# Kernel tuning notes

Hardware: AMD Instinct MI355X
Metric: run time of the kernel (lower is better)

The kernel has to match this reference:

```python
import jax, jax.numpy as jnp
import numpy as np

B, T, D, H = 2, 2048, 1024, 16
DH = D // H  # 64


def setup_inputs() -> dict:
    key = jax.random.key(0)
    ks = jax.random.split(key, 6)
    s = 1.0 / np.sqrt(D)
    return {
        "x": jax.random.normal(ks[0], (B, T, D), dtype=jnp.float32),
        "Wq": jax.random.normal(ks[1], (D, D), dtype=jnp.float32) * s,
        "Wk": jax.random.normal(ks[2], (D, D), dtype=jnp.float32) * s,
        "Wv": jax.random.normal(ks[3], (D, D), dtype=jnp.float32) * s,
        "Wo": jax.random.normal(ks[4], (D, D), dtype=jnp.float32) * s,
        "bo": jnp.zeros((D,), dtype=jnp.float32),
    }


def reference(x, Wq, Wk, Wv, Wo, bo):
    b, t, _ = x.shape
    # projections (torch Linear: x @ W.T; here W stored as [d_in, d_out])
    q = (x @ Wq).reshape(b, t, H, DH).transpose(0, 2, 1, 3)  # [b,H,t,dh]
    k = (x @ Wk).reshape(b, t, H, DH).transpose(0, 2, 1, 3)
    v = (x @ Wv).reshape(b, t, H, DH).transpose(0, 2, 1, 3)
    scores = jnp.einsum("bhqd,bhkd->bhqk", q, k) / np.sqrt(DH).astype(np.float32)
    causal = jnp.tril(jnp.ones((t, t), dtype=bool))  # True = keep
    scores = jnp.where(causal, scores, -jnp.inf)
    weights = jax.nn.softmax(scores, axis=-1)
    ctx = jnp.einsum("bhqk,bhkd->bhqd", weights, v)
    ctx = ctx.transpose(0, 2, 1, 3).reshape(b, t, D)
    return ctx @ Wo + bo
```

## Files before the change

kernel.cpp:

```cpp
#include <hip/hip_runtime.h>


typedef unsigned short u16;
typedef __attribute__((ext_vector_type(8))) short short8;
typedef __attribute__((ext_vector_type(4))) short short4_t;
typedef __attribute__((ext_vector_type(4))) float f32x4;

#define B_ 2
#define T_ 2048
#define D_ 1024
#define H_ 16
#define DH_ 64
#define M_ (B_ * T_)
#define SCALE_LOG2E 0.18033688011112042f
#define NEG_BIG -3.0e4f

#define GLOAD16(g, l)                                                     \
  __builtin_amdgcn_global_load_lds(                                       \
      (const __attribute__((address_space(1))) void*)(g),                 \
      (__attribute__((address_space(3))) void*)(l), 16, 0, 0)

__device__ __forceinline__ u16 f2bf(float f) {
  union { float f; unsigned u; } v; v.f = f;
  unsigned r = v.u + 0x7fffu + ((v.u >> 16) & 1u);
  return (u16)(r >> 16);
}
__device__ __forceinline__ u16 f2bf_trunc(float f) {
  union { float f; unsigned u; } v; v.f = f;
  return (u16)(v.u >> 16);
}
__device__ __forceinline__ float exp2_raw(float x) {
  float r;
  asm volatile("v_exp_f32 %0, %1" : "=v"(r) : "v"(x));
  return r;
}

__global__ __launch_bounds__(256) void cvt_x(const float* __restrict__ x,
                                             u16* __restrict__ xb) {
  const int i = (blockIdx.x * 256 + threadIdx.x) * 8;
  float4 a = *(const float4*)(x + i);
  float4 b = *(const float4*)(x + i + 4);
  short8 o;
  o[0] = (short)f2bf(a.x); o[1] = (short)f2bf(a.y);
  o[2] = (short)f2bf(a.z); o[3] = (short)f2bf(a.w);
  o[4] = (short)f2bf(b.x); o[5] = (short)f2bf(b.y);
  o[6] = (short)f2bf(b.z); o[7] = (short)f2bf(b.w);
  *(short8*)(xb + i) = o;
}

__global__ __launch_bounds__(256) void transpose_w(
    const float* __restrict__ w0, const float* __restrict__ w1,
    const float* __restrict__ w2, const float* __restrict__ w3,
    u16* __restrict__ outT) {
  __shared__ u16 Tl[64][72];
  const int z = blockIdx.z;
  const float* src = (z == 0) ? w0 : (z == 1) ? w1 : (z == 2) ? w2 : w3;
  const int r0 = blockIdx.y * 64, c0 = blockIdx.x * 64;
  const int tid = threadIdx.x;
  const int rr = tid >> 2, cc = (tid & 3) * 16;

  const float* p = src + (size_t)(r0 + rr) * D_ + c0 + cc;
  float4 f0 = *(const float4*)p;
  float4 f1 = *(const float4*)(p + 4);
  float4 f2 = *(const float4*)(p + 8);
  float4 f3 = *(const float4*)(p + 12);
  Tl[rr][cc + 0] = f2bf(f0.x); Tl[rr][cc + 1] = f2bf(f0.y);
  Tl[rr][cc + 2] = f2bf(f0.z); Tl[rr][cc + 3] = f2bf(f0.w);
  Tl[rr][cc + 4] = f2bf(f1.x); Tl[rr][cc + 5] = f2bf(f1.y);
  Tl[rr][cc + 6] = f2bf(f1.z); Tl[rr][cc + 7] = f2bf(f1.w);
  Tl[rr][cc + 8] = f2bf(f2.x); Tl[rr][cc + 9] = f2bf(f2.y);
  Tl[rr][cc +10] = f2bf(f2.z); Tl[rr][cc +11] = f2bf(f2.w);
  Tl[rr][cc +12] = f2bf(f3.x); Tl[rr][cc +13] = f2bf(f3.y);
  Tl[rr][cc +14] = f2bf(f3.z); Tl[rr][cc +15] = f2bf(f3.w);
  __syncthreads();

  u16* o = outT + (size_t)z * D_ * D_ + (size_t)(c0 + rr) * D_ + r0 + cc;
  short8 x0, x1;
#pragma unroll
  for (int i = 0; i < 8; i++) x0[i] = (short)Tl[cc + i][rr];
#pragma unroll
  for (int i = 0; i < 8; i++) x1[i] = (short)Tl[cc + 8 + i][rr];
  *(short8*)o = x0;
  *(short8*)(o + 8) = x1;
}

__global__ __launch_bounds__(256) void qkv_gemm(
    const u16* __restrict__ x, const u16* __restrict__ wT,
    u16* __restrict__ qkv) {
  __shared__ u16 As[128][32];
  __shared__ u16 Bs[128][32];

  const int z = blockIdx.z;
  const u16* W = wT + (size_t)z * D_ * D_;
  u16* out = qkv + (size_t)z * M_ * D_;
  const int n0 = blockIdx.x * 128;
  const int m0 = blockIdx.y * 128;
  const int tid = threadIdx.x;
  const int lane = tid & 63, w = tid >> 6;
  const int quad = lane >> 4, l16 = lane & 15;
  const int wr = w >> 1, wc = w & 1;

  f32x4 acc[4][4] = {};
  const int grow = w * 16 + (lane >> 2);
  const int gcol = (lane & 3) * 8;
  u16* lA = (u16*)As + w * 512;
  u16* lB = (u16*)Bs + w * 512;

  for (int k0 = 0; k0 < D_; k0 += 32) {
    const u16* gA = x + (size_t)(m0 + grow) * D_ + k0 + gcol;
    const u16* gB = W + (size_t)(n0 + grow) * D_ + k0 + gcol;
    GLOAD16(gA, lA);
    GLOAD16(gA + (size_t)64 * D_, lA + 2048);
    GLOAD16(gB, lB);
    GLOAD16(gB + (size_t)64 * D_, lB + 2048);
    __syncthreads();

    short8 af[4], bf[4];
#pragma unroll
    for (int i = 0; i < 4; i++)
      af[i] = *(const short8*)&As[wr * 64 + i * 16 + l16][quad * 8];
#pragma unroll
    for (int i = 0; i < 4; i++)
      bf[i] = *(const short8*)&Bs[wc * 64 + i * 16 + l16][quad * 8];
#pragma unroll
    for (int i = 0; i < 4; i++)
#pragma unroll
      for (int j = 0; j < 4; j++)
        acc[i][j] = __builtin_amdgcn_mfma_f32_16x16x32_bf16(af[i], bf[j], acc[i][j], 0, 0, 0);
    __syncthreads();
  }

  const float osc = (z == 0) ? SCALE_LOG2E : 1.0f;
#pragma unroll
  for (int i = 0; i < 4; i++) {
#pragma unroll
    for (int j = 0; j < 4; j++) {
      const int n = n0 + wc * 64 + j * 16 + l16;
      const int h = n >> 6, dh = n & 63;
#pragma unroll
      for (int r = 0; r < 4; r++) {
        const int m = m0 + wr * 64 + i * 16 + quad * 4 + r;
        const int b = m >> 11, t = m & (T_ - 1);
        out[(((size_t)(b * H_ + h)) * T_ + t) * DH_ + dh] = f2bf(acc[i][j][r] * osc);
      }
    }
  }
}

__global__ __launch_bounds__(256) void transpose_v(
    const u16* __restrict__ v, u16* __restrict__ vT) {
  __shared__ u16 Tl[64][72];
  const int t0 = blockIdx.x * 64;
  const int bh = blockIdx.y;
  const int tid = threadIdx.x;
  const int rr = tid >> 2, cc = (tid & 3) * 16;

  const u16* p = v + (size_t)bh * T_ * DH_ + (size_t)(t0 + rr) * DH_ + cc;
  short8 a0 = *(const short8*)p;
  short8 a1 = *(const short8*)(p + 8);
  *(short8*)&Tl[rr][cc] = a0;
  *(short8*)&Tl[rr][cc + 8] = a1;
  __syncthreads();

  u16* o = vT + (size_t)bh * DH_ * T_ + (size_t)rr * T_ + t0 + cc;
  short8 x0, x1;
#pragma unroll
  for (int i = 0; i < 8; i++) x0[i] = (short)Tl[cc + i][rr];
#pragma unroll
  for (int i = 0; i < 8; i++) x1[i] = (short)Tl[cc + 8 + i][rr];
  *(short8*)o = x0;
  *(short8*)(o + 8) = x1;
}

__global__ __launch_bounds__(128) void attn(
    const u16* __restrict__ qg, const u16* __restrict__ kg,
    const u16* __restrict__ vtg, u16* __restrict__ ctx) {
  __shared__ u16 Ks[64][72];
  __shared__ u16 Vs[64][72];
  __shared__ u16 Ps[2][2][16][72];

  const int qt = gridDim.x - 1 - blockIdx.x;
  const int bh = blockIdx.y;
  const int tid = threadIdx.x;
  const int w = tid >> 6, lane = tid & 63;
  const int quad = lane >> 4, l16 = lane & 15;
  const int q0 = qt * 64;
  const size_t baseQK = (size_t)bh * T_ * DH_;
  const size_t baseV  = (size_t)bh * DH_ * T_;

  const int qrowA = q0 + w * 32 + l16;
  const int qrowB = qrowA + 16;
  short8 qfA0 = *(const short8*)(qg + baseQK + (size_t)qrowA * DH_ + quad * 8);
  short8 qfA1 = *(const short8*)(qg + baseQK + (size_t)qrowA * DH_ + 32 + quad * 8);
  short8 qfB0 = *(const short8*)(qg + baseQK + (size_t)qrowB * DH_ + quad * 8);
  short8 qfB1 = *(const short8*)(qg + baseQK + (size_t)qrowB * DH_ + 32 + quad * 8);

  f32x4 oaccA[4] = {}, oaccB[4] = {};
  float liA = 0.f, liB = 0.f;

  const int srow = tid >> 1;
  const int scol = (tid & 1) * 32;

  const u16* kp = kg + baseQK + (size_t)srow * DH_ + scol;
  const u16* vp = vtg + baseV + (size_t)srow * T_ + scol;
  short8 kr0 = *(const short8*)kp;
  short8 kr1 = *(const short8*)(kp + 8);
  short8 kr2 = *(const short8*)(kp + 16);
  short8 kr3 = *(const short8*)(kp + 24);
  short8 vr0 = *(const short8*)vp;
  short8 vr1 = *(const short8*)(vp + 8);
  short8 vr2 = *(const short8*)(vp + 16);
  short8 vr3 = *(const short8*)(vp + 24);

  for (int kv0 = 0; kv0 <= q0; kv0 += 64) {
    __syncthreads();
    *(short8*)&Ks[srow][scol]      = kr0;
    *(short8*)&Ks[srow][scol + 8]  = kr1;
    *(short8*)&Ks[srow][scol + 16] = kr2;
    *(short8*)&Ks[srow][scol + 24] = kr3;
    *(short8*)&Vs[srow][scol]      = vr0;
    *(short8*)&Vs[srow][scol + 8]  = vr1;
    *(short8*)&Vs[srow][scol + 16] = vr2;
    *(short8*)&Vs[srow][scol + 24] = vr3;
    if (kv0 < q0) {
      const u16* kn = kg + baseQK + (size_t)(kv0 + 64 + srow) * DH_ + scol;
      const u16* vn = vtg + baseV + (size_t)srow * T_ + kv0 + 64 + scol;
      kr0 = *(const short8*)kn;
      kr1 = *(const short8*)(kn + 8);
      kr2 = *(const short8*)(kn + 16);
      kr3 = *(const short8*)(kn + 24);
      vr0 = *(const short8*)vn;
      vr1 = *(const short8*)(vn + 8);
      vr2 = *(const short8*)(vn + 16);
      vr3 = *(const short8*)(vn + 24);
    }
    __syncthreads();

    short8 kf0[4], kf1[4];
#pragma unroll
    for (int cb = 0; cb < 4; cb++) {
      kf0[cb] = *(const short8*)&Ks[cb * 16 + l16][quad * 8];
      kf1[cb] = *(const short8*)&Ks[cb * 16 + l16][32 + quad * 8];
    }

    f32x4 svA[4], svB[4];
#pragma unroll
    for (int cb = 0; cb < 4; cb++) {
      f32x4 z = {};
      svA[cb] = __builtin_amdgcn_mfma_f32_16x16x32_bf16(kf0[cb], qfA0, z, 0, 0, 0);
      svA[cb] = __builtin_amdgcn_mfma_f32_16x16x32_bf16(kf1[cb], qfA1, svA[cb], 0, 0, 0);
      svB[cb] = __builtin_amdgcn_mfma_f32_16x16x32_bf16(kf0[cb], qfB0, z, 0, 0, 0);
      svB[cb] = __builtin_amdgcn_mfma_f32_16x16x32_bf16(kf1[cb], qfB1, svB[cb], 0, 0, 0);
    }

    float pA[4][4], pB[4][4];
    if (kv0 == q0) {
#pragma unroll
      for (int cb = 0; cb < 4; cb++)
#pragma unroll
        for (int r = 0; r < 4; r++) {
          const int kv = kv0 + cb * 16 + quad * 4 + r;
          pA[cb][r] = exp2_raw((kv <= qrowA) ? svA[cb][r] : NEG_BIG);
          pB[cb][r] = exp2_raw((kv <= qrowB) ? svB[cb][r] : NEG_BIG);
        }
    } else {
#pragma unroll
      for (int cb = 0; cb < 4; cb++)
#pragma unroll
        for (int r = 0; r < 4; r++) {
          pA[cb][r] = exp2_raw(svA[cb][r]);
          pB[cb][r] = exp2_raw(svB[cb][r]);
        }
    }
#pragma unroll
    for (int cb = 0; cb < 4; cb++)
#pragma unroll
      for (int r = 0; r < 4; r++) { liA += pA[cb][r]; liB += pB[cb][r]; }

    short8 vf0[4], vf1[4];
#pragma unroll
    for (int cb = 0; cb < 4; cb++) {
      vf0[cb] = *(const short8*)&Vs[cb * 16 + l16][quad * 8];
      vf1[cb] = *(const short8*)&Vs[cb * 16 + l16][32 + quad * 8];
    }

#pragma unroll
    for (int cb = 0; cb < 4; cb++) {
      short4_t pkA, pkB;
#pragma unroll
      for (int r = 0; r < 4; r++) {
        pkA[r] = (short)f2bf_trunc(pA[cb][r]);
        pkB[r] = (short)f2bf_trunc(pB[cb][r]);
      }
      *(short4_t*)&Ps[w][0][l16][cb * 16 + quad * 4] = pkA;
      *(short4_t*)&Ps[w][1][l16][cb * 16 + quad * 4] = pkB;
    }
    short8 paA0 = *(const short8*)&Ps[w][0][l16][quad * 8];
    short8 paA1 = *(const short8*)&Ps[w][0][l16][32 + quad * 8];
    short8 paB0 = *(const short8*)&Ps[w][1][l16][quad * 8];
    short8 paB1 = *(const short8*)&Ps[w][1][l16][32 + quad * 8];
#pragma unroll
    for (int cb = 0; cb < 4; cb++) {
      oaccA[cb] = __builtin_amdgcn_mfma_f32_16x16x32_bf16(vf0[cb], paA0, oaccA[cb], 0, 0, 0);
      oaccA[cb] = __builtin_amdgcn_mfma_f32_16x16x32_bf16(vf1[cb], paA1, oaccA[cb], 0, 0, 0);
      oaccB[cb] = __builtin_amdgcn_mfma_f32_16x16x32_bf16(vf0[cb], paB0, oaccB[cb], 0, 0, 0);
      oaccB[cb] = __builtin_amdgcn_mfma_f32_16x16x32_bf16(vf1[cb], paB1, oaccB[cb], 0, 0, 0);
    }
  }

  liA += __shfl_xor(liA, 16, 64); liA += __shfl_xor(liA, 32, 64);
  liB += __shfl_xor(liB, 16, 64); liB += __shfl_xor(liB, 32, 64);
  const int b = bh >> 4, h = bh & 15;
  const float invA = 1.0f / liA, invB = 1.0f / liB;
  u16* outA = ctx + ((size_t)(b * T_ + qrowA)) * D_ + h * 64 + quad * 4;
  u16* outB = ctx + ((size_t)(b * T_ + qrowB)) * D_ + h * 64 + quad * 4;
#pragma unroll
  for (int cb = 0; cb < 4; cb++) {
    short4_t oA, oB;
#pragma unroll
    for (int r = 0; r < 4; r++) {
      oA[r] = (short)f2bf(oaccA[cb][r] * invA);
      oB[r] = (short)f2bf(oaccB[cb][r] * invB);
    }
    *(short4_t*)(outA + cb * 16) = oA;
    *(short4_t*)(outB + cb * 16) = oB;
  }
}

__global__ __launch_bounds__(256) void out_gemm(
    const u16* __restrict__ ctx, const u16* __restrict__ woT,
    const float* __restrict__ bo, float* __restrict__ out) {
  __shared__ u16 As[64][32];
  __shared__ u16 Bs[128][32];

  const int n0 = blockIdx.x * 128;
  const int m0 = blockIdx.y * 64;
  const int tid = threadIdx.x;
  const int lane = tid & 63, w = tid >> 6;
  const int quad = lane >> 4, l16 = lane & 15;
  const int wr = w >> 1, wc = w & 1;

  f32x4 acc[2][4] = {};
  const int grow = w * 16 + (lane >> 2);
  const int gcol = (lane & 3) * 8;
  u16* lA = (u16*)As + w * 512;
  u16* lB = (u16*)Bs + w * 512;

  for (int k0 = 0; k0 < D_; k0 += 32) {
    const u16* gA = ctx + (size_t)(m0 + grow) * D_ + k0 + gcol;
    const u16* gB = woT + (size_t)(n0 + grow) * D_ + k0 + gcol;
    GLOAD16(gA, lA);
    GLOAD16(gB, lB);
    GLOAD16(gB + (size_t)64 * D_, lB + 2048);
    __syncthreads();

    short8 af[2], bf[4];
#pragma unroll
    for (int i = 0; i < 2; i++)
      af[i] = *(const short8*)&As[wr * 32 + i * 16 + l16][quad * 8];
#pragma unroll
    for (int i = 0; i < 4; i++)
      bf[i] = *(const short8*)&Bs[wc * 64 + i * 16 + l16][quad * 8];
#pragma unroll
    for (int i = 0; i < 2; i++)
#pragma unroll
      for (int j = 0; j < 4; j++)
        acc[i][j] = __builtin_amdgcn_mfma_f32_16x16x32_bf16(af[i], bf[j], acc[i][j], 0, 0, 0);
    __syncthreads();
  }

#pragma unroll
  for (int i = 0; i < 2; i++) {
#pragma unroll
    for (int j = 0; j < 4; j++) {
      const int n = n0 + wc * 64 + j * 16 + l16;
      const float bias = bo[n];
#pragma unroll
      for (int r = 0; r < 4; r++) {
        const int m = m0 + wr * 32 + i * 16 + quad * 4 + r;
        out[(size_t)m * D_ + n] = acc[i][j][r] + bias;
      }
    }
  }
}

extern "C" void kernel_launch(void* const* d_in, const int* in_sizes, int n_in,
                              void* d_out, int out_size, void* d_ws, size_t ws_size,
                              hipStream_t stream) {
  const float* x  = (const float*)d_in[0];
  const float* Wq = (const float*)d_in[1];
  const float* Wk = (const float*)d_in[2];
  const float* Wv = (const float*)d_in[3];
  const float* Wo = (const float*)d_in[4];
  const float* bo = (const float*)d_in[5];
  float* out = (float*)d_out;

  u16* ws  = (u16*)d_ws;
  u16* xb  = ws;
  u16* wT  = xb + (size_t)M_ * D_;
  u16* qkv = wT + (size_t)4 * D_ * D_;
  u16* ctx = qkv + (size_t)3 * M_ * D_;
  u16* vT  = xb;

  cvt_x<<<dim3(M_ * D_ / (256 * 8)), 256, 0, stream>>>(x, xb);
  transpose_w<<<dim3(16, 16, 4), 256, 0, stream>>>(Wq, Wk, Wv, Wo, wT);
  qkv_gemm<<<dim3(D_ / 128, M_ / 128, 3), 256, 0, stream>>>(xb, wT, qkv);
  transpose_v<<<dim3(T_ / 64, B_ * H_), 256, 0, stream>>>(qkv + (size_t)2 * M_ * D_, vT);
  attn<<<dim3(T_ / 64, B_ * H_), 128, 0, stream>>>(
      qkv, qkv + (size_t)M_ * D_, vT, ctx);
  out_gemm<<<dim3(D_ / 128, M_ / 64), 256, 0, stream>>>(ctx, wT + (size_t)3 * D_ * D_, bo, out);
}
```

Baseline: 203.5 us.

## Split long causal attention query tiles across KV chunks with a combine pass

Query tiles with longer causal KV ranges are split into 1–4 KV chunks, each handled by its own block. The blocks write unnormalized fp32 partial outputs and row sums to workspace, and a separate combine kernel sums and normalizes them. This aims to fix load imbalance and the low block count (only 1024 blocks of 128 threads, with very uneven work) in the causal attention kernel. In exchange it adds an extra launch and fp32 partial traffic. It also relies on a fixed max without running-max rescaling, which is already assumed by the base. It falls back to the monolithic kernel if the workspace is too small.

Result: faster. 198.1 us (-2.7%).

```diff
diff --git a/kernel.cpp b/kernel.cpp
--- a/kernel.cpp
+++ b/kernel.cpp
@@ -14,6 +14,11 @@
 #define M_ (B_ * T_)
 #define SCALE_LOG2E 0.18033688011112042f
 #define NEG_BIG -3.0e4f
+
+#define SLOT_F 4160
+#define SLOTS_PER_BH 72
+#define OPART_BYTES ((size_t)32 * SLOTS_PER_BH * SLOT_F * 4)
+#define WS_BASE_BYTES ((size_t)24 * 1024 * 1024 * 2)
 
 #define GLOAD16(g, l)                                                     \
   __builtin_amdgcn_global_load_lds(                                       \
@@ -172,7 +177,242 @@
   *(short8*)(o + 8) = x1;
 }
 
-__global__ __launch_bounds__(128) void attn(
+__device__ __forceinline__ int slot_base(int qt) {
+  return (qt < 16) ? (qt - 8) * 2
+       : (qt < 24) ? 16 + (qt - 16) * 3
+                   : 40 + (qt - 24) * 4;
+}
+
+__global__ __launch_bounds__(128) void attn_chunk(
+    const u16* __restrict__ qg, const u16* __restrict__ kg,
+    const u16* __restrict__ vtg, u16* __restrict__ ctx,
+    float* __restrict__ Opart) {
+  __shared__ u16 Ks[64][72];
+  __shared__ u16 Vs[64][72];
+  __shared__ u16 Ps[2][2][16][72];
+
+  const int cid = 79 - blockIdx.x;
+  int qt, c, nc;
+  if (cid < 8)       { qt = cid;                    c = 0;               nc = 1; }
+  else if (cid < 24) { qt = 8  + ((cid - 8) >> 1);  c = (cid - 8) & 1;   nc = 2; }
+  else if (cid < 48) { qt = 16 + (cid - 24) / 3;    c = (cid - 24) % 3;  nc = 3; }
+  else               { qt = 24 + ((cid - 48) >> 2); c = (cid - 48) & 3;  nc = 4; }
+  const int nt = qt + 1;
+  const int kv_lo = (c * nt / nc) * 64;
+  const int kv_hi = ((c + 1) * nt / nc) * 64;
+  const int q0 = qt * 64;
+
+  const int bh = blockIdx.y;
+  const int tid = threadIdx.x;
+  const int w = tid >> 6, lane = tid & 63;
+  const int quad = lane >> 4, l16 = lane & 15;
+  const size_t baseQK = (size_t)bh * T_ * DH_;
+  const size_t baseV  = (size_t)bh * DH_ * T_;
+
+  const int qrowA = q0 + w * 32 + l16;
+  const int qrowB = qrowA + 16;
+  short8 qfA0 = *(const short8*)(qg + baseQK + (size_t)qrowA * DH_ + quad * 8);
+  short8 qfA1 = *(const short8*)(qg + baseQK + (size_t)qrowA * DH_ + 32 + quad * 8);
+  short8 qfB0 = *(const short8*)(qg + baseQK + (size_t)qrowB * DH_ + quad * 8);
+  short8 qfB1 = *(const short8*)(qg + baseQK + (size_t)qrowB * DH_ + 32 + quad * 8);
+
+  f32x4 oaccA[4] = {}, oaccB[4] = {};
+  float liA = 0.f, liB = 0.f;
+
+  const int srow = tid >> 1;
+  const int scol = (tid & 1) * 32;
+
+  const u16* kp = kg + baseQK + (size_t)(kv_lo + srow) * DH_ + scol;
+  const u16* vp = vtg + baseV + (size_t)srow * T_ + kv_lo + scol;
+  short8 kr0 = *(const short8*)kp;
+  short8 kr1 = *(const short8*)(kp + 8);
+  short8 kr2 = *(const short8*)(kp + 16);
+  short8 kr3 = *(const short8*)(kp + 24);
+  short8 vr0 = *(const short8*)vp;
+  short8 vr1 = *(const short8*)(vp + 8);
+  short8 vr2 = *(const short8*)(vp + 16);
+  short8 vr3 = *(const short8*)(vp + 24);
+
+  for (int kv0 = kv_lo; kv0 < kv_hi; kv0 += 64) {
+    __syncthreads();
+    *(short8*)&Ks[srow][scol]      = kr0;
+    *(short8*)&Ks[srow][scol + 8]  = kr1;
+    *(short8*)&Ks[srow][scol + 16] = kr2;
+    *(short8*)&Ks[srow][scol + 24] = kr3;
+    *(short8*)&Vs[srow][scol]      = vr0;
+    *(short8*)&Vs[srow][scol + 8]  = vr1;
+    *(short8*)&Vs[srow][scol + 16] = vr2;
+    *(short8*)&Vs[srow][scol + 24] = vr3;
+    if (kv0 + 64 < kv_hi) {
+      const u16* kn = kg + baseQK + (size_t)(kv0 + 64 + srow) * DH_ + scol;
+      const u16* vn = vtg + baseV + (size_t)srow * T_ + kv0 + 64 + scol;
+      kr0 = *(const short8*)kn;
+      kr1 = *(const short8*)(kn + 8);
+      kr2 = *(const short8*)(kn + 16);
+      kr3 = *(const short8*)(kn + 24);
+      vr0 = *(const short8*)vn;
+      vr1 = *(const short8*)(vn + 8);
+      vr2 = *(const short8*)(vn + 16);
+      vr3 = *(const short8*)(vn + 24);
+    }
+    __syncthreads();
+
+    short8 kf0[4], kf1[4];
+#pragma unroll
+    for (int cb = 0; cb < 4; cb++) {
+      kf0[cb] = *(const short8*)&Ks[cb * 16 + l16][quad * 8];
+      kf1[cb] = *(const short8*)&Ks[cb * 16 + l16][32 + quad * 8];
+    }
+
+    f32x4 svA[4], svB[4];
+    __builtin_amdgcn_s_setprio(1);
+#pragma unroll
+    for (int cb = 0; cb < 4; cb++) {
+      f32x4 z = {};
+      svA[cb] = __builtin_amdgcn_mfma_f32_16x16x32_bf16(kf0[cb], qfA0, z, 0, 0, 0);
+      svA[cb] = __builtin_amdgcn_mfma_f32_16x16x32_bf16(kf1[cb], qfA1, svA[cb], 0, 0, 0);
+      svB[cb] = __builtin_amdgcn_mfma_f32_16x16x32_bf16(kf0[cb], qfB0, z, 0, 0, 0);
+      svB[cb] = __builtin_amdgcn_mfma_f32_16x16x32_bf16(kf1[cb], qfB1, svB[cb], 0, 0, 0);
+    }
+    __builtin_amdgcn_s_setprio(0);
+
+    float pA[4][4], pB[4][4];
+    if (kv0 == q0) {
+#pragma unroll
+      for (int cb = 0; cb < 4; cb++)
+#pragma unroll
+        for (int r = 0; r < 4; r++) {
+          const int kv = kv0 + cb * 16 + quad * 4 + r;
+          pA[cb][r] = exp2_raw((kv <= qrowA) ? svA[cb][r] : NEG_BIG);
+          pB[cb][r] = exp2_raw((kv <= qrowB) ? svB[cb][r] : NEG_BIG);
+        }
+    } else {
+#pragma unroll
+      for (int cb = 0; cb < 4; cb++)
+#pragma unroll
+        for (int r = 0; r < 4; r++) {
+          pA[cb][r] = exp2_raw(svA[cb][r]);
+          pB[cb][r] = exp2_raw(svB[cb][r]);
+        }
+    }
+#pragma unroll
+    for (int cb = 0; cb < 4; cb++)
+#pragma unroll
+      for (int r = 0; r < 4; r++) { liA += pA[cb][r]; liB += pB[cb][r]; }
+
+    short8 vf0[4], vf1[4];
+#pragma unroll
+    for (int cb = 0; cb < 4; cb++) {
+      vf0[cb] = *(const short8*)&Vs[cb * 16 + l16][quad * 8];
+      vf1[cb] = *(const short8*)&Vs[cb * 16 + l16][32 + quad * 8];
+    }
+
+#pragma unroll
+    for (int cb = 0; cb < 4; cb++) {
+      short4_t pkA, pkB;
+#pragma unroll
+      for (int r = 0; r < 4; r++) {
+        pkA[r] = (short)f2bf_trunc(pA[cb][r]);
+        pkB[r] = (short)f2bf_trunc(pB[cb][r]);
+      }
+      *(short4_t*)&Ps[w][0][l16][cb * 16 + quad * 4] = pkA;
+      *(short4_t*)&Ps[w][1][l16][cb * 16 + quad * 4] = pkB;
+    }
+    short8 paA0 = *(const short8*)&Ps[w][0][l16][quad * 8];
+    short8 paA1 = *(const short8*)&Ps[w][0][l16][32 + quad * 8];
+    short8 paB0 = *(const short8*)&Ps[w][1][l16][quad * 8];
+    short8 paB1 = *(const short8*)&Ps[w][1][l16][32 + quad * 8];
+    __builtin_amdgcn_s_setprio(1);
+#pragma unroll
+    for (int cb = 0; cb < 4; cb++) {
+      oaccA[cb] = __builtin_amdgcn_mfma_f32_16x16x32_bf16(vf0[cb], paA0, oaccA[cb], 0, 0, 0);
+      oaccA[cb] = __builtin_amdgcn_mfma_f32_16x16x32_bf16(vf1[cb], paA1, oaccA[cb], 0, 0, 0);
+      oaccB[cb] = __builtin_amdgcn_mfma_f32_16x16x32_bf16(vf0[cb], paB0, oaccB[cb], 0, 0, 0);
+      oaccB[cb] = __builtin_amdgcn_mfma_f32_16x16x32_bf16(vf1[cb], paB1, oaccB[cb], 0, 0, 0);
+    }
+    __builtin_amdgcn_s_setprio(0);
+  }
+
+  liA += __shfl_xor(liA, 16, 64); liA += __shfl_xor(liA, 32, 64);
+  liB += __shfl_xor(liB, 16, 64); liB += __shfl_xor(liB, 32, 64);
+
+  if (nc == 1) {
+    const int b = bh >> 4, h = bh & 15;
+    const float invA = 1.0f / liA, invB = 1.0f / liB;
+    u16* outA = ctx + ((size_t)(b * T_ + qrowA)) * D_ + h * 64 + quad * 4;
+    u16* outB = ctx + ((size_t)(b * T_ + qrowB)) * D_ + h * 64 + quad * 4;
+#pragma unroll
+    for (int cb = 0; cb < 4; cb++) {
+      short4_t oA, oB;
+#pragma unroll
+      for (int r = 0; r < 4; r++) {
+        oA[r] = (short)f2bf(oaccA[cb][r] * invA);
+        oB[r] = (short)f2bf(oaccB[cb][r] * invB);
+      }
+      *(short4_t*)(outA + cb * 16) = oA;
+      *(short4_t*)(outB + cb * 16) = oB;
+    }
+  } else {
+    float* slot = Opart + ((size_t)bh * SLOTS_PER_BH + slot_base(qt) + c) * SLOT_F;
+    float* pA = slot + (size_t)(w * 32 + l16) * 64 + quad * 4;
+    float* pB = slot + (size_t)(w * 32 + 16 + l16) * 64 + quad * 4;
+#pragma unroll
+    for (int cb = 0; cb < 4; cb++) {
+      *(f32x4*)(pA + cb * 16) = oaccA[cb];
+      *(f32x4*)(pB + cb * 16) = oaccB[cb];
+    }
+    if (quad == 0) {
+      slot[4096 + w * 32 + l16] = liA;
+      slot[4096 + w * 32 + 16 + l16] = liB;
+    }
+  }
+}
+
+__global__ __launch_bounds__(256) void attn_combine(
+    const float* __restrict__ Opart, u16* __restrict__ ctx) {
+  __shared__ float ls[64];
+  const int qt = blockIdx.x + 8;
+  const int bh = blockIdx.y;
+  const int nc = 1 + (qt >> 3);
+  const float* slot0 = Opart + ((size_t)bh * SLOTS_PER_BH + slot_base(qt)) * SLOT_F;
+  const int tid = threadIdx.x;
+
+  if (tid < 64) {
+    float s = 0.f;
+    for (int c = 0; c < nc; c++) s += slot0[(size_t)c * SLOT_F + 4096 + tid];
+    ls[tid] = 1.0f / s;
+  }
+  __syncthreads();
+
+  const int q = tid >> 2, d0 = (tid & 3) * 16;
+  const float* p = slot0 + (size_t)q * 64 + d0;
+  f32x4 a0 = *(const f32x4*)(p);
+  f32x4 a1 = *(const f32x4*)(p + 4);
+  f32x4 a2 = *(const f32x4*)(p + 8);
+  f32x4 a3 = *(const f32x4*)(p + 12);
+  for (int c = 1; c < nc; c++) {
+    const float* pc = p + (size_t)c * SLOT_F;
+    a0 += *(const f32x4*)(pc);
+    a1 += *(const f32x4*)(pc + 4);
+    a2 += *(const f32x4*)(pc + 8);
+    a3 += *(const f32x4*)(pc + 12);
+  }
+  const float inv = ls[q];
+  short8 o0, o1;
+#pragma unroll
+  for (int i = 0; i < 4; i++) {
+    o0[i]     = (short)f2bf(a0[i] * inv);
+    o0[i + 4] = (short)f2bf(a1[i] * inv);
+    o1[i]     = (short)f2bf(a2[i] * inv);
+    o1[i + 4] = (short)f2bf(a3[i] * inv);
+  }
+  const int b = bh >> 4, h = bh & 15;
+  u16* op = ctx + ((size_t)(b * T_ + qt * 64 + q)) * D_ + h * 64 + d0;
+  *(short8*)op = o0;
+  *(short8*)(op + 8) = o1;
+}
+
+__global__ __launch_bounds__(128) void attn_mono(
     const u16* __restrict__ qg, const u16* __restrict__ kg,
     const u16* __restrict__ vtg, u16* __restrict__ ctx) {
   __shared__ u16 Ks[64][72];
@@ -401,12 +641,21 @@
   u16* qkv = wT + (size_t)4 * D_ * D_;
   u16* ctx = qkv + (size_t)3 * M_ * D_;
   u16* vT  = xb;
+  float* Opart = (float*)(ctx + (size_t)M_ * D_);
 
   cvt_x<<<dim3(M_ * D_ / (256 * 8)), 256, 0, stream>>>(x, xb);
   transpose_w<<<dim3(16, 16, 4), 256, 0, stream>>>(Wq, Wk, Wv, Wo, wT);
   qkv_gemm<<<dim3(D_ / 128, M_ / 128, 3), 256, 0, stream>>>(xb, wT, qkv);
   transpose_v<<<dim3(T_ / 64, B_ * H_), 256, 0, stream>>>(qkv + (size_t)2 * M_ * D_, vT);
-  attn<<<dim3(T_ / 64, B_ * H_), 128, 0, stream>>>(
-      qkv, qkv + (size_t)M_ * D_, vT, ctx);
+
+  if (ws_size >= WS_BASE_BYTES + OPART_BYTES) {
+    attn_chunk<<<dim3(80, B_ * H_), 128, 0, stream>>>(
+        qkv, qkv + (size_t)M_ * D_, vT, ctx, Opart);
+    attn_combine<<<dim3(24, B_ * H_), 256, 0, stream>>>(Opart, ctx);
+  } else {
+    attn_mono<<<dim3(T_ / 64, B_ * H_), 128, 0, stream>>>(
+        qkv, qkv + (size_t)M_ * D_, vT, ctx);
+  }
+
   out_gemm<<<dim3(D_ / 128, M_ / 64), 256, 0, stream>>>(ctx, wT + (size_t)3 * D_ * D_, bo, out);
 }
```
